# Performance work log

Measured on AMD Instinct MI355X. Metric: run time of the kernel, lower is better.

Reference implementation:

```python
import jax, jax.numpy as jnp
import numpy as np
from functools import partial

BN_EPS = 1e-5

def conv1d(x, w, b):
    # x: [B,Cin,L], w: [Cout,Cin,3], padding=1
    y = jax.lax.conv_general_dilated(x, w, window_strides=(1,), padding=[(1, 1)],
                                     dimension_numbers=('NCH', 'OIH', 'NCH'))
    return y + b[None, :, None]

def bn_eval(x, bn):
    # bn: [4, C] rows = (scale, bias, mean, var); x: [B,C,L]
    scale, bias, mean, var = bn[0], bn[1], bn[2], bn[3]
    inv = scale / jnp.sqrt(var + BN_EPS)
    return x * inv[None, :, None] + (bias - mean * inv)[None, :, None]

def cbr(x, w, b, bn):
    return jax.nn.relu(bn_eval(conv1d(x, w, b), bn))

def expert_fwd(emb, w1, b1, bn1, w2, b2, bn2, w3, b3, bn3):
    h = cbr(emb, w1, b1, bn1)          # [B,64,L]
    h = cbr(h, w2, b2, bn2)            # [B,32,L]
    h = cbr(h, w3, b3, bn3)            # [B,16,L]
    return jnp.max(h, axis=-1)         # AdaptiveMaxPool1d(1) -> [B,16]

def _bn_pack(rng, c):
    return jnp.asarray(np.stack([1.0 + 0.1 * rng.standard_normal(c),
                                 0.1 * rng.standard_normal(c),
                                 0.1 * rng.standard_normal(c),
                                 rng.uniform(0.5, 1.5, c)]), dtype=jnp.float32)

def setup_inputs() -> dict:
    rng = np.random.default_rng(0)
    B, L, V, D, E = 16384, 60, 64, 128, 3
    g = lambda *s: jnp.asarray(0.05 * rng.standard_normal(s), dtype=jnp.float32)
    emb_table = np.asarray(rng.standard_normal((V, D)), dtype=np.float32) * 0.1
    emb_table[0] = 0.0  # padding_idx=0
    inp = {
        'x': jnp.asarray(rng.integers(0, V, (B, L)), dtype=jnp.int64),
        'emb_table': jnp.asarray(emb_table),
        'g_conv_w': g(64, D, 3), 'g_conv_b': g(64), 'g_bn': _bn_pack(rng, 64),
        'g_fc1_w': g(32, 64), 'g_fc1_b': g(32),
        'g_fc2_w': g(E, 32), 'g_fc2_b': g(E),
        'e_conv1_w': g(E, 64, D, 3), 'e_conv1_b': g(E, 64),
        'e_bn1': jnp.stack([_bn_pack(rng, 64) for _ in range(E)]),
        'e_conv2_w': g(E, 32, 64, 3), 'e_conv2_b': g(E, 32),
        'e_bn2': jnp.stack([_bn_pack(rng, 32) for _ in range(E)]),
        'e_conv3_w': g(E, 16, 32, 3), 'e_conv3_b': g(E, 16),
        'e_bn3': jnp.stack([_bn_pack(rng, 16) for _ in range(E)]),
        'fc1_w': g(64, 16), 'fc1_b': g(64),
        'fc2_w': g(2, 64), 'fc2_b': g(2),
    }
    return inp

def reference(x, emb_table, g_conv_w, g_conv_b, g_bn, g_fc1_w, g_fc1_b,
              g_fc2_w, g_fc2_b, e_conv1_w, e_conv1_b, e_bn1, e_conv2_w,
              e_conv2_b, e_bn2, e_conv3_w, e_conv3_b, e_bn3, fc1_w, fc1_b,
              fc2_w, fc2_b):
    E = e_conv1_w.shape[0]
    emb = jnp.transpose(emb_table[x], (0, 2, 1))           # [B,D,L]
    # gating: conv+bn+relu -> global max pool -> 2-layer MLP -> softmax -> top-1
    h = jnp.max(cbr(emb, g_conv_w, g_conv_b, g_bn), axis=-1)   # [B,64]
    glogits = jax.nn.relu(h @ g_fc1_w.T + g_fc1_b) @ g_fc2_w.T + g_fc2_b
    gates = jax.nn.softmax(glogits, axis=-1)               # [B,E]
    top_idx = jnp.argmax(gates, axis=-1)                   # [B]
    # dense dispatch: compute all experts, mask-accumulate (training path)
    outs = jax.vmap(expert_fwd, in_axes=(None,) + (0,) * 9)(
        emb, e_conv1_w, e_conv1_b, e_bn1, e_conv2_w, e_conv2_b, e_bn2,
        e_conv3_w, e_conv3_b, e_bn3)                       # [E,B,16]
    onehot = jax.nn.one_hot(top_idx, E, dtype=outs.dtype)  # [B,E]
    expert_out = jnp.einsum('be,ebc->bc', onehot, outs)    # [B,16]
    out = jax.nn.relu(expert_out @ fc1_w.T + fc1_b)        # [B,64]
    logits = out @ fc2_w.T + fc2_b                         # [B,2]
    return logits
```

## Files before the change

### kernel.cpp

```cpp
#include <hip/hip_runtime.h>
#include <math.h>

#define BN_EPS 1e-5f

typedef float v2f __attribute__((ext_vector_type(2)));

__device__ __align__(16) float g_wgT[24576 + 192];
__device__ __align__(16) float g_we2T[18432 + 96];
__device__ __align__(16) float g_we3T[4608 + 48];

__device__ __align__(16) float g_P[12480];
__device__ __align__(16) float e_P[37440];
__device__ float g_bninv[64], g_bnadd[64];
__device__ float e1_inv[192], e1_add[192];
__device__ float c2_inv[96], c2_add[96];
__device__ float c3_inv[48], c3_add[48];

__global__ __launch_bounds__(256) void transpose_w_kernel(
    const float* __restrict__ gw, const float* __restrict__ e2w,
    const float* __restrict__ e3w) {
  int idx = blockIdx.x * 256 + threadIdx.x;
  if (idx < 24576) {
    int co = idx & 63, r = idx >> 6;
    int t = r % 3, ci = r / 3;
    g_wgT[idx] = gw[(co * 128 + ci) * 3 + t];
  } else if (idx < 24576 + 18432) {
    int jj = idx - 24576;
    int e = jj / 6144, j = jj % 6144;
    int co = j & 31, r = j >> 5;
    int t = r % 3, ci = r / 3;
    g_we2T[jj] = e2w[e * 6144 + (co * 64 + ci) * 3 + t];
  } else if (idx < 24576 + 18432 + 4608) {
    int jj = idx - (24576 + 18432);
    int e = jj / 1536, j = jj % 1536;
    int co = j & 15, r = j >> 4;
    int t = r % 3, ci = r / 3;
    g_we3T[jj] = e3w[e * 1536 + (co * 32 + ci) * 3 + t];
  }
}

__global__ __launch_bounds__(256) void build_p_kernel(
    const float* __restrict__ embt, const float* __restrict__ gw,
    const float* __restrict__ e1w, const float* __restrict__ gbn,
    const float* __restrict__ gcb, const float* __restrict__ ebn1,
    const float* __restrict__ e1b, const float* __restrict__ ebn2,
    const float* __restrict__ e2b, const float* __restrict__ ebn3,
    const float* __restrict__ e3b) {
  int idx = blockIdx.x * 256 + threadIdx.x;
  if (idx < 12480) {
    int co = idx & 63, r = idx >> 6;
    int v = r % 65, t = r / 65;
    float a = 0.f;
    if (v < 64) {
#pragma unroll 8
      for (int ci = 0; ci < 128; ++ci)
        a = fmaf(embt[v * 128 + ci], gw[(co * 128 + ci) * 3 + t], a);
    }
    g_P[idx] = a;
  } else if (idx < 12480 + 37440) {
    int j = idx - 12480;
    int co = j & 63, r = j >> 6;
    int v = r % 65, tt = r / 65;
    int t = tt % 3, e = tt / 3;
    float a = 0.f;
    if (v < 64) {
#pragma unroll 8
      for (int ci = 0; ci < 128; ++ci)
        a = fmaf(embt[v * 128 + ci], e1w[e * 24576 + (co * 128 + ci) * 3 + t],
                 a);
    }
    e_P[j] = a;
  } else if (idx < 12480 + 37440 + 400) {
    int q = idx - (12480 + 37440);
    if (q < 64) {
      int co = q;
      float inv = gbn[co] / sqrtf(gbn[192 + co] + BN_EPS);
      g_bninv[co] = inv;
      g_bnadd[co] = gbn[64 + co] + (gcb[co] - gbn[128 + co]) * inv;
    } else if (q < 256) {
      int j = q - 64;
      int e = j >> 6, co = j & 63;
      const float* bn = ebn1 + e * 256;
      float inv = bn[co] / sqrtf(bn[192 + co] + BN_EPS);
      e1_inv[j] = inv;
      e1_add[j] = bn[64 + co] + (e1b[e * 64 + co] - bn[128 + co]) * inv;
    } else if (q < 352) {
      int j = q - 256;
      int e = j >> 5, co = j & 31;
      const float* bn = ebn2 + e * 128;
      float inv = bn[co] / sqrtf(bn[96 + co] + BN_EPS);
      c2_inv[j] = inv;
      c2_add[j] = bn[32 + co] + (e2b[e * 32 + co] - bn[64 + co]) * inv;
    } else {
      int j = q - 352;
      int e = j >> 4, co = j & 15;
      const float* bn = ebn3 + e * 64;
      float inv = bn[co] / sqrtf(bn[48 + co] + BN_EPS);
      c3_inv[j] = inv;
      c3_add[j] = bn[16 + co] + (e3b[e * 16 + co] - bn[32 + co]) * inv;
    }
  }
}

template <int CIN, int CO, int NCO>
__device__ __forceinline__ void convG(const float* __restrict__ wT,
                                      const float* E, int l,
                                      v2f (&acc)[NCO / 2]) {
#pragma unroll 4
  for (int ci = 0; ci < CIN; ++ci) {
    const float* row = E + ci * 64 + l;
    float e0 = row[0], e1 = row[1], e2 = row[2];
    v2f e0v = {e0, e0}, e1v = {e1, e1}, e2v = {e2, e2};
    const float* wrow = wT + ci * (3 * CO);
#pragma unroll
    for (int k2 = 0; k2 < NCO / 2; ++k2) {
      v2f w0 = *reinterpret_cast<const v2f*>(wrow + 2 * k2);
      v2f w1 = *reinterpret_cast<const v2f*>(wrow + CO + 2 * k2);
      v2f w2 = *reinterpret_cast<const v2f*>(wrow + 2 * CO + 2 * k2);
      acc[k2] = __builtin_elementwise_fma(
          e0v, w0,
          __builtin_elementwise_fma(
              e1v, w1, __builtin_elementwise_fma(e2v, w2, acc[k2])));
    }
  }
}

template <int CIN, int CO, int NCO>
__device__ __forceinline__ void convA(const float* __restrict__ wT,
                                      const float* E, int l,
                                      v2f (&A0)[NCO / 2], v2f (&A1)[NCO / 2],
                                      v2f (&A2)[NCO / 2]) {
#pragma unroll 2
  for (int ci = 0; ci < CIN; ++ci) {
    float r = E[ci * 64 + l];
    v2f rv = {r, r};
    const float* wrow = wT + ci * (3 * CO);
#pragma unroll
    for (int k2 = 0; k2 < NCO / 2; ++k2) {
      v2f w0 = *reinterpret_cast<const v2f*>(wrow + 2 * k2);
      v2f w1 = *reinterpret_cast<const v2f*>(wrow + CO + 2 * k2);
      v2f w2 = *reinterpret_cast<const v2f*>(wrow + 2 * CO + 2 * k2);
      A0[k2] = __builtin_elementwise_fma(rv, w0, A0[k2]);
      A1[k2] = __builtin_elementwise_fma(rv, w1, A1[k2]);
      A2[k2] = __builtin_elementwise_fma(rv, w2, A2[k2]);
    }
  }
}

__global__ __launch_bounds__(256, 8) void moe_fused_kernel(
    const int* __restrict__ x, const float* __restrict__ embt,
    const float* __restrict__ gcb, const float* __restrict__ gbn,
    const float* __restrict__ gf1w, const float* __restrict__ gf1b,
    const float* __restrict__ gf2w, const float* __restrict__ gf2b,
    const float* __restrict__ f1w, const float* __restrict__ f1b,
    const float* __restrict__ f2w, const float* __restrict__ f2b,
    float* __restrict__ out) {
  __shared__ __align__(16) float smem[4608];
  float* Bbuf = smem;
  float* Gbuf = smem;
  float* Cbuf = smem + 2048;
  float* Pbuf = smem + 4160;
  float* hbuf = smem + 4416;
  float* h2buf = smem + 4480;
  float* glog = smem + 4512;
  float* mbuf = smem + 4516;
  float* o64 = smem + 4532;
  __shared__ int toks[64];
  __shared__ int selbuf, fbflag;

  const int b = blockIdx.x;
  const int tid = threadIdx.x;
  const int lane = tid & 63;
  const int wv = tid >> 6;
  const int wvu = __builtin_amdgcn_readfirstlane(wv);
  const bool valid = (lane < 60);
  const int cob = wvu * 16;
  const int wcol = (lane == 63) ? 0 : lane + 1;

  if (tid < 64) toks[tid] = x[b * 60 + (tid < 60 ? tid : 59)];
  __syncthreads();

  auto table_sum = [&](const float* __restrict__ P, float(&s)[16]) {
    const int l = lane;
    const int v0 = l ? toks[l - 1] : 64;
    const int v1 = toks[l];
    const int v2 = (l < 59) ? toks[l + 1] : 64;
    const float4* r0 = reinterpret_cast<const float4*>(P + v0 * 64 + cob);
    const float4* r1 =
        reinterpret_cast<const float4*>(P + 4160 + v1 * 64 + cob);
    const float4* r2 =
        reinterpret_cast<const float4*>(P + 8320 + v2 * 64 + cob);
#pragma unroll
    for (int q = 0; q < 4; ++q) {
      float4 a0 = r0[q], a1 = r1[q], a2 = r2[q];
      s[4 * q + 0] = (a1.x + a0.x) + a2.x;
      s[4 * q + 1] = (a1.y + a0.y) + a2.y;
      s[4 * q + 2] = (a1.z + a0.z) + a2.z;
      s[4 * q + 3] = (a1.w + a0.w) + a2.w;
    }
  };

  {
    float s[16];
    table_sum(g_P, s);
#pragma unroll
    for (int k = 0; k < 16; ++k) {
      int co = cob + k;
      float v =
          valid ? fmaxf(fmaf(s[k], g_bninv[co], g_bnadd[co]), 0.f) : 0.f;
      Gbuf[lane * 65 + co] = v;
    }
  }
  __syncthreads();
  {
    const int ch = tid & 63, q = tid >> 6;
    const float* col = Gbuf + (q * 15) * 65 + ch;
    float m = col[0];
#pragma unroll
    for (int i = 1; i < 15; ++i) m = fmaxf(m, col[i * 65]);
    Pbuf[q * 64 + ch] = m;
  }
  __syncthreads();
  if (tid < 64)
    hbuf[tid] = fmaxf(fmaxf(Pbuf[tid], Pbuf[64 + tid]),
                      fmaxf(Pbuf[128 + tid], Pbuf[192 + tid]));
  __syncthreads();

  {
    const int o = tid >> 3, p = tid & 7;
    const float* wrow = gf1w + o * 64 + p * 8;
    float4 wa = reinterpret_cast<const float4*>(wrow)[0];
    float4 wb = reinterpret_cast<const float4*>(wrow)[1];
    const float* hh = hbuf + p * 8;
    float a = 0.f;
    a = fmaf(hh[0], wa.x, a);
    a = fmaf(hh[1], wa.y, a);
    a = fmaf(hh[2], wa.z, a);
    a = fmaf(hh[3], wa.w, a);
    a = fmaf(hh[4], wb.x, a);
    a = fmaf(hh[5], wb.y, a);
    a = fmaf(hh[6], wb.z, a);
    a = fmaf(hh[7], wb.w, a);
    a += __shfl_xor(a, 1, 64);
    a += __shfl_xor(a, 2, 64);
    a += __shfl_xor(a, 4, 64);
    if (p == 0) h2buf[o] = fmaxf(a + gf1b[o], 0.f);
  }
  __syncthreads();
  if (tid < 3) {
    float a = gf2b[tid];
#pragma unroll 8
    for (int k = 0; k < 32; ++k) a = fmaf(h2buf[k], gf2w[tid * 32 + k], a);
    glog[tid] = a;
  }
  __syncthreads();
  if (tid == 0) {
    int best = 0;
    float bv = glog[0];
    if (glog[1] > bv) { bv = glog[1]; best = 1; }
    if (glog[2] > bv) { bv = glog[2]; best = 2; }
    float second = -1e30f;
#pragma unroll
    for (int i = 0; i < 3; ++i)
      if (i != best) second = fmaxf(second, glog[i]);
    selbuf = best;
    fbflag = (bv - second < 2e-4f) ? 1 : 0;
  }
  __syncthreads();

  if (fbflag) {
    float* tileF = smem;
    float* TbufF = smem + 2048;
    if (tid < 128) {
      int r = tid >> 2;
      const int ctab[4] = {0, 61, 62, 63};
      tileF[r * 64 + ctab[tid & 3]] = 0.f;
    }
    v2f acc[8] = {};
    for (int tile = 0; tile < 4; ++tile) {
      for (int i = tid; i < 60 * 32; i += 256) {
        int l = i >> 5, dp = i & 31;
        TbufF[l * 33 + dp] = embt[toks[l] * 128 + tile * 32 + dp];
      }
      __syncthreads();
      if (valid) {
#pragma unroll
        for (int dp = wvu; dp < 32; dp += 4)
          tileF[dp * 64 + lane + 1] = TbufF[lane * 33 + dp];
      }
      __syncthreads();
      convG<32, 64, 16>(g_wgT + tile * 32 * 192 + cob, tileF, lane, acc);
      __syncthreads();
    }
#pragma unroll
    for (int k = 0; k < 16; ++k) {
      int co = cob + k;
      float inv = gbn[co] / sqrtf(gbn[192 + co] + BN_EPS);
      float add = gbn[64 + co] + (gcb[co] - gbn[128 + co]) * inv;
      float v = valid ? fmaxf(fmaf(acc[k >> 1][k & 1], inv, add), 0.f) : 0.f;
#pragma unroll
      for (int off = 1; off < 64; off <<= 1)
        v = fmaxf(v, __shfl_xor(v, off, 64));
      if (lane == 0) hbuf[co] = v;
    }
    __syncthreads();
    if (tid < 32) {
      float a = gf1b[tid];
#pragma unroll 8
      for (int k = 0; k < 64; ++k) a = fmaf(hbuf[k], gf1w[tid * 64 + k], a);
      h2buf[tid] = fmaxf(a, 0.f);
    }
    __syncthreads();
    if (tid < 3) {
      float a = gf2b[tid];
#pragma unroll 8
      for (int k = 0; k < 32; ++k) a = fmaf(h2buf[k], gf2w[tid * 32 + k], a);
      glog[tid] = a;
    }
    __syncthreads();
    if (tid == 0) {
      int best = 0;
      float bv = glog[0];
      if (glog[1] > bv) { bv = glog[1]; best = 1; }
      if (glog[2] > bv) { best = 2; }
      selbuf = best;
    }
    __syncthreads();
  }
  const int e = __builtin_amdgcn_readfirstlane(selbuf);

  {
    float s[16];
    table_sum(e_P + e * 12480, s);
#pragma unroll
    for (int k = 0; k < 16; ++k) {
      int co = cob + k;
      float vv =
          fmaxf(fmaf(s[k], e1_inv[e * 64 + co], e1_add[e * 64 + co]), 0.f);
      Bbuf[co * 64 + wcol] = valid ? vv : 0.f;
    }
  }
  __syncthreads();

  {
    v2f A0[4] = {}, A1[4] = {}, A2[4] = {};
    const int cob2 = wvu * 8;
    convA<64, 32, 8>(g_we2T + e * 6144 + cob2, Bbuf, lane, A0, A1, A2);
    float val8[8];
#pragma unroll
    for (int k = 0; k < 8; ++k) {
      int co = cob2 + k;
      float a1 = __shfl(A1[k >> 1][k & 1], lane + 1, 64);
      float a2 = __shfl(A2[k >> 1][k & 1], lane + 2, 64);
      float ss = (A0[k >> 1][k & 1] + a1) + a2;
      float vv =
          fmaxf(fmaf(ss, c2_inv[e * 32 + co], c2_add[e * 32 + co]), 0.f);
      val8[k] = valid ? vv : 0.f;
    }
    __syncthreads();
#pragma unroll
    for (int k = 0; k < 8; ++k) Bbuf[(cob2 + k) * 64 + wcol] = val8[k];
  }
  __syncthreads();

  {
    v2f A0[2] = {}, A1[2] = {}, A2[2] = {};
    const int cob3 = wvu * 4;
    convA<32, 16, 4>(g_we3T + e * 1536 + cob3, Bbuf, lane, A0, A1, A2);
#pragma unroll
    for (int k = 0; k < 4; ++k) {
      int co = cob3 + k;
      float a1 = __shfl(A1[k >> 1][k & 1], lane + 1, 64);
      float a2 = __shfl(A2[k >> 1][k & 1], lane + 2, 64);
      float ss = (A0[k >> 1][k & 1] + a1) + a2;
      float v = valid ? fmaxf(fmaf(ss, c3_inv[e * 16 + co],
                                   c3_add[e * 16 + co]), 0.f)
                      : 0.f;
      if (valid) Cbuf[lane * 17 + co] = v;
    }
  }
  __syncthreads();
  if (tid < 64) {
    const int ch = tid & 15, q = tid >> 4;
    const float* col = Cbuf + (q * 15) * 17 + ch;
    float m = col[0];
#pragma unroll
    for (int i = 1; i < 15; ++i) m = fmaxf(m, col[i * 17]);
    Pbuf[q * 16 + ch] = m;
  }
  __syncthreads();
  if (tid < 16)
    mbuf[tid] = fmaxf(fmaxf(Pbuf[tid], Pbuf[16 + tid]),
                      fmaxf(Pbuf[32 + tid], Pbuf[48 + tid]));
  __syncthreads();

  if (tid < 64) {
    float a = f1b[tid];
#pragma unroll
    for (int k = 0; k < 16; ++k) a = fmaf(mbuf[k], f1w[tid * 16 + k], a);
    o64[tid] = fmaxf(a, 0.f);
  }
  __syncthreads();
  if (tid < 128) {
    const int o = tid >> 6, j = tid & 63;
    float a = o64[j] * f2w[o * 64 + j];
    a += __shfl_xor(a, 1, 64);
    a += __shfl_xor(a, 2, 64);
    a += __shfl_xor(a, 4, 64);
    a += __shfl_xor(a, 8, 64);
    a += __shfl_xor(a, 16, 64);
    a += __shfl_xor(a, 32, 64);
    if (j == 0) out[b * 2 + o] = a + f2b[o];
  }
}

extern "C" void kernel_launch(void* const* d_in, const int* in_sizes, int n_in,
                              void* d_out, int out_size, void* d_ws,
                              size_t ws_size, hipStream_t stream) {
  const int* x = (const int*)d_in[0];
  const float* embt = (const float*)d_in[1];
  const float* gcw = (const float*)d_in[2];
  const float* gcb = (const float*)d_in[3];
  const float* gbn = (const float*)d_in[4];
  const float* gf1w = (const float*)d_in[5];
  const float* gf1b = (const float*)d_in[6];
  const float* gf2w = (const float*)d_in[7];
  const float* gf2b = (const float*)d_in[8];
  const float* e1w = (const float*)d_in[9];
  const float* e1b = (const float*)d_in[10];
  const float* ebn1 = (const float*)d_in[11];
  const float* e2w = (const float*)d_in[12];
  const float* e2b = (const float*)d_in[13];
  const float* ebn2 = (const float*)d_in[14];
  const float* e3w = (const float*)d_in[15];
  const float* e3b = (const float*)d_in[16];
  const float* ebn3 = (const float*)d_in[17];
  const float* f1w = (const float*)d_in[18];
  const float* f1b = (const float*)d_in[19];
  const float* f2w = (const float*)d_in[20];
  const float* f2b = (const float*)d_in[21];
  float* out = (float*)d_out;

  const int B = in_sizes[0] / 60;

  transpose_w_kernel<<<(47616 + 255) / 256, 256, 0, stream>>>(gcw, e2w, e3w);
  build_p_kernel<<<(50320 + 255) / 256, 256, 0, stream>>>(
      embt, gcw, e1w, gbn, gcb, ebn1, e1b, ebn2, e2b, ebn3, e3b);
  moe_fused_kernel<<<B, 256, 0, stream>>>(x, embt, gcb, gbn, gf1w, gf1b, gf2w,
                                          gf2b, f1w, f1b, f2w, f2b, out);
}
```

Before: 331.5 us.

## Store precomputed conv tables in fp16 and fold BN scale into weights

The per-token conv lookup tables for the gating and first expert layers are stored in half precision, so each table-sum gather reads half as many bytes. BatchNorm scale and shift are folded into the tables and into the transposed layer-2/3 weights, which removes the per-channel scale loads and FMAs in the fused kernel. The gating fc2 is now a 96-thread shuffle reduction, and the near-tie fallback threshold is widened to cover the extra fp16 rounding. The cost is lower accuracy in the first-layer activations, which could flip top-1 expert choices near ties and shift outputs.

```diff
diff --git a/kernel.cpp b/kernel.cpp
--- a/kernel.cpp
+++ b/kernel.cpp
@@ -1,4 +1,5 @@
 #include <hip/hip_runtime.h>
+#include <hip/hip_fp16.h>
 #include <math.h>
 
 #define BN_EPS 1e-5f
@@ -9,16 +10,14 @@
 __device__ __align__(16) float g_we2T[18432 + 96];
 __device__ __align__(16) float g_we3T[4608 + 48];
 
-__device__ __align__(16) float g_P[12480];
-__device__ __align__(16) float e_P[37440];
-__device__ float g_bninv[64], g_bnadd[64];
-__device__ float e1_inv[192], e1_add[192];
-__device__ float c2_inv[96], c2_add[96];
-__device__ float c3_inv[48], c3_add[48];
+__device__ __align__(16) __half g_Ph[12480];
+__device__ __align__(16) __half e_Ph[37440];
+__device__ float c2_add[96], c3_add[48];
 
 __global__ __launch_bounds__(256) void transpose_w_kernel(
     const float* __restrict__ gw, const float* __restrict__ e2w,
-    const float* __restrict__ e3w) {
+    const float* __restrict__ e3w, const float* __restrict__ ebn2,
+    const float* __restrict__ ebn3) {
   int idx = blockIdx.x * 256 + threadIdx.x;
   if (idx < 24576) {
     int co = idx & 63, r = idx >> 6;
@@ -29,13 +28,17 @@
     int e = jj / 6144, j = jj % 6144;
     int co = j & 31, r = j >> 5;
     int t = r % 3, ci = r / 3;
-    g_we2T[jj] = e2w[e * 6144 + (co * 64 + ci) * 3 + t];
+    const float* bn = ebn2 + e * 128;
+    float inv = bn[co] / sqrtf(bn[96 + co] + BN_EPS);
+    g_we2T[jj] = e2w[e * 6144 + (co * 64 + ci) * 3 + t] * inv;
   } else if (idx < 24576 + 18432 + 4608) {
     int jj = idx - (24576 + 18432);
     int e = jj / 1536, j = jj % 1536;
     int co = j & 15, r = j >> 4;
     int t = r % 3, ci = r / 3;
-    g_we3T[jj] = e3w[e * 1536 + (co * 32 + ci) * 3 + t];
+    const float* bn = ebn3 + e * 64;
+    float inv = bn[co] / sqrtf(bn[48 + co] + BN_EPS);
+    g_we3T[jj] = e3w[e * 1536 + (co * 32 + ci) * 3 + t] * inv;
   }
 }
 
@@ -52,11 +55,15 @@
     int v = r % 65, t = r / 65;
     float a = 0.f;
     if (v < 64) {
+      float dot = 0.f;
 #pragma unroll 8
       for (int ci = 0; ci < 128; ++ci)
-        a = fmaf(embt[v * 128 + ci], gw[(co * 128 + ci) * 3 + t], a);
-    }
-    g_P[idx] = a;
+        dot = fmaf(embt[v * 128 + ci], gw[(co * 128 + ci) * 3 + t], dot);
+      float inv = gbn[co] / sqrtf(gbn[192 + co] + BN_EPS);
+      float add = gbn[64 + co] + (gcb[co] - gbn[128 + co]) * inv;
+      a = (t == 1) ? fmaf(dot, inv, add) : dot * inv;
+    }
+    g_Ph[idx] = __float2half(a);
   } else if (idx < 12480 + 37440) {
     int j = idx - 12480;
     int co = j & 63, r = j >> 6;
@@ -64,39 +71,29 @@
     int t = tt % 3, e = tt / 3;
     float a = 0.f;
     if (v < 64) {
+      float dot = 0.f;
 #pragma unroll 8
       for (int ci = 0; ci < 128; ++ci)
-        a = fmaf(embt[v * 128 + ci], e1w[e * 24576 + (co * 128 + ci) * 3 + t],
-                 a);
-    }
-    e_P[j] = a;
-  } else if (idx < 12480 + 37440 + 400) {
-    int q = idx - (12480 + 37440);
-    if (q < 64) {
-      int co = q;
-      float inv = gbn[co] / sqrtf(gbn[192 + co] + BN_EPS);
-      g_bninv[co] = inv;
-      g_bnadd[co] = gbn[64 + co] + (gcb[co] - gbn[128 + co]) * inv;
-    } else if (q < 256) {
-      int j = q - 64;
-      int e = j >> 6, co = j & 63;
+        dot = fmaf(embt[v * 128 + ci],
+                   e1w[e * 24576 + (co * 128 + ci) * 3 + t], dot);
       const float* bn = ebn1 + e * 256;
       float inv = bn[co] / sqrtf(bn[192 + co] + BN_EPS);
-      e1_inv[j] = inv;
-      e1_add[j] = bn[64 + co] + (e1b[e * 64 + co] - bn[128 + co]) * inv;
-    } else if (q < 352) {
-      int j = q - 256;
-      int e = j >> 5, co = j & 31;
+      float add = bn[64 + co] + (e1b[e * 64 + co] - bn[128 + co]) * inv;
+      a = (t == 1) ? fmaf(dot, inv, add) : dot * inv;
+    }
+    e_Ph[j] = __float2half(a);
+  } else if (idx < 12480 + 37440 + 144) {
+    int q = idx - (12480 + 37440);
+    if (q < 96) {
+      int e = q >> 5, co = q & 31;
       const float* bn = ebn2 + e * 128;
       float inv = bn[co] / sqrtf(bn[96 + co] + BN_EPS);
-      c2_inv[j] = inv;
-      c2_add[j] = bn[32 + co] + (e2b[e * 32 + co] - bn[64 + co]) * inv;
+      c2_add[q] = bn[32 + co] + (e2b[e * 32 + co] - bn[64 + co]) * inv;
     } else {
-      int j = q - 352;
+      int j = q - 96;
       int e = j >> 4, co = j & 15;
       const float* bn = ebn3 + e * 64;
       float inv = bn[co] / sqrtf(bn[48 + co] + BN_EPS);
-      c3_inv[j] = inv;
       c3_add[j] = bn[16 + co] + (e3b[e * 16 + co] - bn[32 + co]) * inv;
     }
   }
@@ -180,35 +177,38 @@
   if (tid < 64) toks[tid] = x[b * 60 + (tid < 60 ? tid : 59)];
   __syncthreads();
 
-  auto table_sum = [&](const float* __restrict__ P, float(&s)[16]) {
+  auto table_sum = [&](const __half* __restrict__ P, float(&s)[16]) {
     const int l = lane;
     const int v0 = l ? toks[l - 1] : 64;
     const int v1 = toks[l];
     const int v2 = (l < 59) ? toks[l + 1] : 64;
-    const float4* r0 = reinterpret_cast<const float4*>(P + v0 * 64 + cob);
-    const float4* r1 =
-        reinterpret_cast<const float4*>(P + 4160 + v1 * 64 + cob);
-    const float4* r2 =
-        reinterpret_cast<const float4*>(P + 8320 + v2 * 64 + cob);
-#pragma unroll
-    for (int q = 0; q < 4; ++q) {
-      float4 a0 = r0[q], a1 = r1[q], a2 = r2[q];
-      s[4 * q + 0] = (a1.x + a0.x) + a2.x;
-      s[4 * q + 1] = (a1.y + a0.y) + a2.y;
-      s[4 * q + 2] = (a1.z + a0.z) + a2.z;
-      s[4 * q + 3] = (a1.w + a0.w) + a2.w;
+    const uint4* r0 = reinterpret_cast<const uint4*>(P + v0 * 64 + cob);
+    const uint4* r1 = reinterpret_cast<const uint4*>(P + 4160 + v1 * 64 + cob);
+    const uint4* r2 = reinterpret_cast<const uint4*>(P + 8320 + v2 * 64 + cob);
+#pragma unroll
+    for (int q = 0; q < 2; ++q) {
+      uint4 u0 = r0[q], u1 = r1[q], u2 = r2[q];
+      const unsigned int a0[4] = {u0.x, u0.y, u0.z, u0.w};
+      const unsigned int a1[4] = {u1.x, u1.y, u1.z, u1.w};
+      const unsigned int a2[4] = {u2.x, u2.y, u2.z, u2.w};
+#pragma unroll
+      for (int w = 0; w < 4; ++w) {
+        float2 f0 = __half22float2(__builtin_bit_cast(__half2, a0[w]));
+        float2 f1 = __half22float2(__builtin_bit_cast(__half2, a1[w]));
+        float2 f2 = __half22float2(__builtin_bit_cast(__half2, a2[w]));
+        s[q * 8 + 2 * w + 0] = (f1.x + f0.x) + f2.x;
+        s[q * 8 + 2 * w + 1] = (f1.y + f0.y) + f2.y;
+      }
     }
   };
 
   {
     float s[16];
-    table_sum(g_P, s);
+    table_sum(g_Ph, s);
 #pragma unroll
     for (int k = 0; k < 16; ++k) {
-      int co = cob + k;
-      float v =
-          valid ? fmaxf(fmaf(s[k], g_bninv[co], g_bnadd[co]), 0.f) : 0.f;
-      Gbuf[lane * 65 + co] = v;
+      float v = valid ? fmaxf(s[k], 0.f) : 0.f;
+      Gbuf[lane * 65 + cob + k] = v;
     }
   }
   __syncthreads();
@@ -247,11 +247,15 @@
     if (p == 0) h2buf[o] = fmaxf(a + gf1b[o], 0.f);
   }
   __syncthreads();
-  if (tid < 3) {
-    float a = gf2b[tid];
-#pragma unroll 8
-    for (int k = 0; k < 32; ++k) a = fmaf(h2buf[k], gf2w[tid * 32 + k], a);
-    glog[tid] = a;
+  if (tid < 96) {
+    const int o = tid >> 5, j = tid & 31;
+    float a = h2buf[j] * gf2w[o * 32 + j];
+    a += __shfl_xor(a, 1, 32);
+    a += __shfl_xor(a, 2, 32);
+    a += __shfl_xor(a, 4, 32);
+    a += __shfl_xor(a, 8, 32);
+    a += __shfl_xor(a, 16, 32);
+    if (j == 0) glog[o] = a + gf2b[o];
   }
   __syncthreads();
   if (tid == 0) {
@@ -264,7 +268,7 @@
     for (int i = 0; i < 3; ++i)
       if (i != best) second = fmaxf(second, glog[i]);
     selbuf = best;
-    fbflag = (bv - second < 2e-4f) ? 1 : 0;
+    fbflag = (bv - second < 5e-4f) ? 1 : 0;
   }
   __syncthreads();
 
@@ -331,13 +335,11 @@
 
   {
     float s[16];
-    table_sum(e_P + e * 12480, s);
+    table_sum(e_Ph + e * 12480, s);
 #pragma unroll
     for (int k = 0; k < 16; ++k) {
-      int co = cob + k;
-      float vv =
-          fmaxf(fmaf(s[k], e1_inv[e * 64 + co], e1_add[e * 64 + co]), 0.f);
-      Bbuf[co * 64 + wcol] = valid ? vv : 0.f;
+      float vv = fmaxf(s[k], 0.f);
+      Bbuf[(cob + k) * 64 + wcol] = valid ? vv : 0.f;
     }
   }
   __syncthreads();
@@ -353,8 +355,7 @@
       float a1 = __shfl(A1[k >> 1][k & 1], lane + 1, 64);
       float a2 = __shfl(A2[k >> 1][k & 1], lane + 2, 64);
       float ss = (A0[k >> 1][k & 1] + a1) + a2;
-      float vv =
-          fmaxf(fmaf(ss, c2_inv[e * 32 + co], c2_add[e * 32 + co]), 0.f);
+      float vv = fmaxf(ss + c2_add[e * 32 + co], 0.f);
       val8[k] = valid ? vv : 0.f;
     }
     __syncthreads();
@@ -373,9 +374,7 @@
       float a1 = __shfl(A1[k >> 1][k & 1], lane + 1, 64);
       float a2 = __shfl(A2[k >> 1][k & 1], lane + 2, 64);
       float ss = (A0[k >> 1][k & 1] + a1) + a2;
-      float v = valid ? fmaxf(fmaf(ss, c3_inv[e * 16 + co],
-                                   c3_add[e * 16 + co]), 0.f)
-                      : 0.f;
+      float v = fmaxf(ss + c3_add[e * 16 + co], 0.f);
       if (valid) Cbuf[lane * 17 + co] = v;
     }
   }
@@ -443,8 +442,9 @@
 
   const int B = in_sizes[0] / 60;
 
-  transpose_w_kernel<<<(47616 + 255) / 256, 256, 0, stream>>>(gcw, e2w, e3w);
-  build_p_kernel<<<(50320 + 255) / 256, 256, 0, stream>>>(
+  transpose_w_kernel<<<(47616 + 255) / 256, 256, 0, stream>>>(gcw, e2w, e3w,
+                                                              ebn2, ebn3);
+  build_p_kernel<<<(50064 + 255) / 256, 256, 0, stream>>>(
       embt, gcw, e1w, gbn, gcb, ebn1, e1b, ebn2, e2b, ebn3, e3b);
   moe_fused_kernel<<<B, 256, 0, stream>>>(x, embt, gcb, gbn, gf1w, gf1b, gf2w,
                                           gf2b, f1w, f1b, f2w, f2b, out);
```

Measured after the change: 339.1 us. 1.02x slower.
